# Performance work log

Hardware: AMD Instinct MI355X
Metric: run time of the kernel (lower is better)

## Reference

```python
import jax, jax.numpy as jnp
import numpy as np

B, S, D, H, DK, DV, W = 2, 8192, 1024, 16, 64, 64, 128


def setup_inputs() -> dict:
    key = jax.random.key(0)
    ks = jax.random.split(key, 5)
    scale = 0.02
    x = jax.random.normal(ks[0], (B, S, D), jnp.float32)
    Wq = jax.random.normal(ks[1], (D, H * DK), jnp.float32) * scale
    Wk = jax.random.normal(ks[2], (D, H * DK), jnp.float32) * scale
    Wv = jax.random.normal(ks[3], (D, H * DV), jnp.float32) * scale
    Wo = jax.random.normal(ks[4], (H * DV, D), jnp.float32) * scale
    return {"x": x, "Wq": Wq, "Wk": Wk, "Wv": Wv, "Wo": Wo, "window_size": W}


def _sliding_window_attn(x, Wq, Wk, Wv, Wo, window_size):
    b, s, d = x.shape
    dk = Wq.shape[1] // H
    dv = Wv.shape[1] // H
    Bq = window_size            # block size == band half-width
    nb = s // Bq                # number of query blocks

    # projections -> [B, H, S, dh]
    q = (x @ Wq).reshape(b, s, H, dk).transpose(0, 2, 1, 3)
    k = (x @ Wk).reshape(b, s, H, dk).transpose(0, 2, 1, 3)
    v = (x @ Wv).reshape(b, s, H, dv).transpose(0, 2, 1, 3)

    qb = q.reshape(b, H, nb, Bq, dk)

    # pad keys/values by one block on each side, gather 3-block local context
    kpad = jnp.pad(k, ((0, 0), (0, 0), (Bq, Bq), (0, 0)))
    vpad = jnp.pad(v, ((0, 0), (0, 0), (Bq, Bq), (0, 0)))
    kb = kpad.reshape(b, H, nb + 2, Bq, dk)
    vb = vpad.reshape(b, H, nb + 2, Bq, dv)
    kctx = jnp.concatenate([kb[:, :, :-2], kb[:, :, 1:-1], kb[:, :, 2:]], axis=3)  # [B,H,nb,3Bq,dk]
    vctx = jnp.concatenate([vb[:, :, :-2], vb[:, :, 1:-1], vb[:, :, 2:]], axis=3)  # [B,H,nb,3Bq,dv]

    scores = jnp.einsum("bhnqd,bhnkd->bhnqk", qb, kctx) / jnp.sqrt(jnp.asarray(dk, x.dtype))

    # banded mask: query global idx i = n*Bq + q_loc; key global idx j = (n-1)*Bq + k_loc
    q_loc = jnp.arange(Bq)[:, None]                 # [Bq,1]
    k_rel = jnp.arange(3 * Bq)[None, :] - Bq        # [1,3Bq], offset of j relative to block start
    band = jnp.abs(k_rel - q_loc) <= window_size    # [Bq,3Bq]
    j_global = jnp.arange(nb)[:, None, None] * Bq + k_rel[None]  # [nb,1,3Bq]
    valid = (j_global >= 0) & (j_global < s)
    mask = band[None] & valid                       # [nb,Bq,3Bq]

    neg = jnp.asarray(-1e9, scores.dtype)
    scores = jnp.where(mask[None, None], scores, neg)
    attn = jax.nn.softmax(scores, axis=-1)

    ctx = jnp.einsum("bhnqk,bhnkd->bhnqd", attn, vctx)           # [B,H,nb,Bq,dv]
    ctx = ctx.reshape(b, H, s, dv).transpose(0, 2, 1, 3).reshape(b, s, H * dv)
    return ctx @ Wo


def reference(x, Wq, Wk, Wv, Wo, window_size):
    return _sliding_window_attn(x, Wq, Wk, Wv, Wo, window_size)
```

## Files before the change

### kernel.cpp

```cpp
#include <hip/hip_runtime.h>


typedef __bf16 bf16_t;
typedef bf16_t bf16x8 __attribute__((ext_vector_type(8)));
typedef bf16_t bf16x4 __attribute__((ext_vector_type(4)));
typedef float f32x4 __attribute__((ext_vector_type(4)));

#define CEXP 0.18033688011112042f

__device__ __forceinline__ f32x4 mfma16(bf16x8 a, bf16x8 b, f32x4 c) {
  return __builtin_amdgcn_mfma_f32_16x16x32_bf16(a, b, c, 0, 0, 0);
}

#define GLL16(gptr, lptr)                                                     \
  __builtin_amdgcn_global_load_lds(                                           \
      (__attribute__((address_space(1))) void*)(gptr),                        \
      (__attribute__((address_space(3))) void*)(lptr), 16, 0, 0)

__global__ __launch_bounds__(256) void prep(const float* __restrict__ x,
                                            const float* __restrict__ W0,
                                            const float* __restrict__ W1,
                                            const float* __restrict__ W2,
                                            const float* __restrict__ W3,
                                            bf16_t* __restrict__ xb,
                                            bf16_t* T0, bf16_t* T1,
                                            bf16_t* T2, bf16_t* T3) {
  __shared__ float tile[32][33];
  const int t = threadIdx.x;
  if (blockIdx.x < 8192) {
    int i = blockIdx.x * 256 + t;
    f32x4 a = *(const f32x4*)&x[(size_t)i * 8];
    f32x4 b = *(const f32x4*)&x[(size_t)i * 8 + 4];
    bf16x8 o;
#pragma unroll
    for (int j = 0; j < 4; ++j) { o[j] = (bf16_t)a[j]; o[4 + j] = (bf16_t)b[j]; }
    *(bf16x8*)&xb[(size_t)i * 8] = o;
    return;
  }
  int wb = blockIdx.x - 8192;
  int z = wb >> 10, rem = wb & 1023;
  int bx = rem & 31, by = rem >> 5;
  const float* W; bf16_t* T;
  switch (z) {
    case 0: W = W0; T = T0; break;
    case 1: W = W1; T = T1; break;
    case 2: W = W2; T = T2; break;
    default: W = W3; T = T3; break;
  }
  int tx = t & 31, ty = t >> 5;
  int xc = bx * 32 + tx;
  int y0 = by * 32;
#pragma unroll
  for (int i = ty; i < 32; i += 8) tile[i][tx] = W[(size_t)(y0 + i) * 1024 + xc];
  __syncthreads();
  int xo = y0 + tx;
  int yo = bx * 32;
#pragma unroll
  for (int i = ty; i < 32; i += 8)
    T[(size_t)(yo + i) * 1024 + xo] = (bf16_t)tile[tx][i];
}

__device__ __forceinline__ void gemm256_loop(const bf16_t* __restrict__ A,
                                             const bf16_t* __restrict__ Bt,
                                             int m0, int n0,
                                             bf16_t (*As)[8192],
                                             bf16_t (*Bs)[8192],
                                             f32x4 acc[8][4]) {
  const int K = 1024, NT = 32;
  const int t = threadIdx.x, l = t & 63, w = t >> 6;
  const int fr = l & 15, quad = l >> 4;
  const int wm = w >> 2, wn = w & 3;
  const int srow = w * 16 + (l >> 2);
  const int scol = ((l & 3) ^ ((l >> 3) & 3)) << 3;
  const bf16_t* Asrc = A + (size_t)(m0 + srow) * K + scol;
  const bf16_t* Bsrc = Bt + (size_t)(n0 + srow) * K + scol;
  const size_t cstep = (size_t)128 * K;
  const int sdst = w * 512 + l * 8;
  const int rdoff = fr * 32 + ((quad ^ ((fr >> 1) & 3)) << 3);
  const int abase = wm * 4096 + rdoff;
  const int bbase = wn * 2048 + rdoff;

#pragma unroll
  for (int tt = 0; tt < 2; ++tt) {
    GLL16(Asrc + tt * 32, &As[tt][sdst]);
    GLL16(Asrc + cstep + tt * 32, &As[tt][4096 + sdst]);
    GLL16(Bsrc + tt * 32, &Bs[tt][sdst]);
    GLL16(Bsrc + cstep + tt * 32, &Bs[tt][4096 + sdst]);
  }
  asm volatile("s_waitcnt vmcnt(4)" ::: "memory");
  __builtin_amdgcn_s_barrier();

  for (int tk = 0; tk < NT; ++tk) {
    const int slot = tk & 3;
    const bf16_t* Ap = As[slot];
    const bf16_t* Bp = Bs[slot];
    const bool st = (tk + 2 < NT);
    const int s2 = (tk + 2) & 3;
    __builtin_amdgcn_sched_barrier(0);
    bf16x8 bq[4], af[4];
#pragma unroll
    for (int j = 0; j < 4; ++j) bq[j] = *(const bf16x8*)&Bp[bbase + j * 512];
#pragma unroll
    for (int i = 0; i < 4; ++i) af[i] = *(const bf16x8*)&Ap[abase + i * 512];
    if (st) {
      GLL16(Asrc + (tk + 2) * 32, &As[s2][sdst]);
      GLL16(Asrc + cstep + (tk + 2) * 32, &As[s2][4096 + sdst]);
    }
    __builtin_amdgcn_s_barrier();
    __builtin_amdgcn_s_setprio(1);
#pragma unroll
    for (int i = 0; i < 4; ++i)
#pragma unroll
      for (int j = 0; j < 4; ++j) acc[i][j] = mfma16(af[i], bq[j], acc[i][j]);
    __builtin_amdgcn_s_setprio(0);
    __builtin_amdgcn_s_barrier();
    __builtin_amdgcn_sched_barrier(0);
#pragma unroll
    for (int i = 0; i < 4; ++i) af[i] = *(const bf16x8*)&Ap[abase + (4 + i) * 512];
    if (st) {
      GLL16(Bsrc + (tk + 2) * 32, &Bs[s2][sdst]);
      GLL16(Bsrc + cstep + (tk + 2) * 32, &Bs[s2][4096 + sdst]);
      asm volatile("s_waitcnt vmcnt(4)" ::: "memory");
    } else {
      asm volatile("s_waitcnt vmcnt(0)" ::: "memory");
    }
    __builtin_amdgcn_s_barrier();
    __builtin_amdgcn_s_setprio(1);
#pragma unroll
    for (int i = 0; i < 4; ++i)
#pragma unroll
      for (int j = 0; j < 4; ++j) acc[4 + i][j] = mfma16(af[i], bq[j], acc[4 + i][j]);
    __builtin_amdgcn_s_setprio(0);
    __builtin_amdgcn_s_barrier();
  }
}

__global__ __launch_bounds__(512, 2) void gemm_qkv(const bf16_t* __restrict__ A,
                                                   const bf16_t* __restrict__ Bt,
                                                   bf16_t* __restrict__ qh,
                                                   bf16_t* __restrict__ kh,
                                                   bf16_t* __restrict__ vT2) {
  __shared__ bf16_t As[4][8192];
  __shared__ bf16_t Bs[4][8192];
  const int id = blockIdx.y * 12 + blockIdx.x;
  const int swz = (id & 7) * 96 + (id >> 3);
  const int m0 = (swz / 12) << 8, n0 = (swz % 12) << 8;

  f32x4 acc[8][4] = {};
  gemm256_loop(A, Bt, m0, n0, As, Bs, acc);

  const int t = threadIdx.x, l = t & 63, w = t >> 6;
  const int fr = l & 15, quad = l >> 4;
  const int wm = w >> 2, wn = w & 3;
  const int colbase = n0 + wn * 64;
  if (colbase < 2048) {
    bf16_t* dst = (colbase < 1024) ? qh : kh;
    const int cb = colbase & 1023;
#pragma unroll
    for (int i = 0; i < 8; ++i)
#pragma unroll
      for (int j = 0; j < 4; ++j) {
        int col = cb + j * 16 + fr;
        int h = col >> 6, dk = col & 63;
#pragma unroll
        for (int r = 0; r < 4; ++r) {
          int cm = m0 + wm * 128 + i * 16 + quad * 4 + r;
          int b = cm >> 13, s = cm & 8191;
          dst[((((size_t)(b * 16 + h) << 13) | s) << 6) | dk] = (bf16_t)acc[i][j][r];
        }
      }
  } else {
    const int cb = colbase - 2048;
#pragma unroll
    for (int i = 0; i < 8; ++i) {
      int s0 = m0 + wm * 128 + i * 16;
      int b = s0 >> 13, sblk = (s0 & 8191) >> 4;
#pragma unroll
      for (int j = 0; j < 4; ++j) {
        int col = cb + j * 16;
        int h = col >> 6, dv = (col & 63) + fr;
        bf16x4 pk;
#pragma unroll
        for (int r = 0; r < 4; ++r) pk[r] = (bf16_t)acc[i][j][r];
        *(bf16x4*)&vT2[((size_t)(b * 16 + h) * 512 + sblk) * 1024 + dv * 16 + quad * 4] = pk;
      }
    }
  }
}

__global__ __launch_bounds__(512, 2) void gemm_bt(const bf16_t* __restrict__ A,
                                                  const bf16_t* __restrict__ Bt,
                                                  float* __restrict__ Cf) {
  __shared__ bf16_t As[4][8192];
  __shared__ bf16_t Bs[4][8192];
  const int id = blockIdx.y * 4 + blockIdx.x;
  const int swz = (id & 7) * 32 + (id >> 3);
  const int m0 = (swz >> 2) << 8, n0 = (swz & 3) << 8;

  f32x4 acc[8][4] = {};
  gemm256_loop(A, Bt, m0, n0, As, Bs, acc);

  const int t = threadIdx.x, l = t & 63, w = t >> 6;
  const int fr = l & 15, quad = l >> 4;
  const int wm = w >> 2, wn = w & 3;
#pragma unroll
  for (int i = 0; i < 8; ++i)
#pragma unroll
    for (int j = 0; j < 4; ++j)
#pragma unroll
      for (int r = 0; r < 4; ++r) {
        int cm = m0 + wm * 128 + i * 16 + quad * 4 + r;
        int cn = n0 + wn * 64 + j * 16 + fr;
        Cf[(size_t)cm * 1024 + cn] = acc[i][j][r];
      }
}

#define SKK 72
#define SVS 136
#define PST 136

__global__ __launch_bounds__(256, 3) void swa(const bf16_t* __restrict__ qh,
                                              const bf16_t* __restrict__ kh,
                                              const bf16_t* __restrict__ vT2,
                                              bf16_t* __restrict__ ctx) {
  __shared__ bf16_t Ks[128 * SKK];
  __shared__ bf16_t Vs[64 * SVS];
  __shared__ bf16_t PsT[4][16 * PST];

  const int t = threadIdx.x, lane = t & 63, w = t >> 6;
  const int n = blockIdx.x, h = blockIdx.y, b = blockIdx.z;
  const int fr = lane & 15, quad = lane >> 4, fk = quad << 3;
  const size_t bh = (size_t)(b * 16 + h);

  bf16x8 aq[2][2];
  {
    const size_t qbase = (bh * 8192 + n * 128 + w * 32) * 64;
#pragma unroll
    for (int qt = 0; qt < 2; ++qt)
#pragma unroll
      for (int ks = 0; ks < 2; ++ks)
        aq[qt][ks] = *(const bf16x8*)&qh[qbase + (size_t)(qt * 16 + fr) * 64 + ks * 32 + fk];
  }

  bf16x8 kr[4], vr[4];
  auto loadKV = [&](int kn) {
#pragma unroll
    for (int it = 0; it < 4; ++it) {
      int c = it * 256 + t;
      kr[it] = *(const bf16x8*)&kh[(bh * 8192 + kn * 128 + (c >> 3)) * 64 + ((c & 7) << 3)];
      int sb = c >> 7, dv = (c & 127) >> 1, sh = c & 1;
      vr[it] = *(const bf16x8*)&vT2[(bh * 512 + kn * 8 + sb) * 1024 + dv * 16 + sh * 8];
    }
  };

  const int cbeg = (n == 0) ? 1 : 0;
  const int cend = (n == 63) ? 1 : 2;
  loadKV(n + cbeg - 1);

  float lrow[2] = {0.f, 0.f};
  f32x4 o[2][4] = {};

  for (int ch = cbeg; ch <= cend; ++ch) {
    __syncthreads();
#pragma unroll
    for (int it = 0; it < 4; ++it) {
      int c = it * 256 + t;
      *(bf16x8*)&Ks[(c >> 3) * SKK + ((c & 7) << 3)] = kr[it];
      int sb = c >> 7, dv = (c & 127) >> 1, sh = c & 1;
      *(bf16x8*)&Vs[dv * SVS + sb * 16 + sh * 8] = vr[it];
    }
    __syncthreads();
    if (ch < cend) loadKV(n + ch);

#pragma unroll
    for (int qt = 0; qt < 2; ++qt) {
      const int lo = (ch == 0) ? 2 * w + qt : 0;
      const int hi = (ch == 2) ? 2 * w + qt : 7;

      f32x4 st[8];
      __builtin_amdgcn_s_setprio(1);
#pragma unroll
      for (int kt = 0; kt < 8; ++kt) {
        if (kt < lo || kt > hi) continue;
        bf16x8 k0 = *(const bf16x8*)&Ks[(kt * 16 + fr) * SKK + fk];
        bf16x8 k1 = *(const bf16x8*)&Ks[(kt * 16 + fr) * SKK + 32 + fk];
        st[kt] = mfma16(k1, aq[qt][1], mfma16(k0, aq[qt][0], (f32x4){0.f, 0.f, 0.f, 0.f}));
      }
      __builtin_amdgcn_s_setprio(0);

#pragma unroll
      for (int kt = 0; kt < 8; ++kt) {
        if (kt < lo || kt > hi) continue;
        const bool dL = (ch == 0) && (kt == lo);
        const bool dR = (ch == 2) && (kt == hi);
        bf16x4 pk;
#pragma unroll
        for (int r = 0; r < 4; ++r) {
          float p = exp2f(st[kt][r] * CEXP);
          int kl = quad * 4 + r;
          if (dL) p = (kl >= fr) ? p : 0.f;
          if (dR) p = (kl <= fr) ? p : 0.f;
          lrow[qt] += p;
          pk[r] = (bf16_t)p;
        }
        *(bf16x4*)&PsT[w][fr * PST + kt * 16 + quad * 4] = pk;
      }
      if ((ch == 0) && (lo & 1)) {
        bf16x4 zz; zz[0] = zz[1] = zz[2] = zz[3] = (bf16_t)0.f;
        *(bf16x4*)&PsT[w][fr * PST + (lo - 1) * 16 + quad * 4] = zz;
      }
      if ((ch == 2) && !(hi & 1)) {
        bf16x4 zz; zz[0] = zz[1] = zz[2] = zz[3] = (bf16_t)0.f;
        *(bf16x4*)&PsT[w][fr * PST + (hi + 1) * 16 + quad * 4] = zz;
      }

      const int pl = lo >> 1, ph = hi >> 1;
      __builtin_amdgcn_s_setprio(1);
#pragma unroll
      for (int ks = 0; ks < 4; ++ks) {
        if (ks < pl || ks > ph) continue;
        bf16x8 pa = *(const bf16x8*)&PsT[w][fr * PST + ks * 32 + fk];
#pragma unroll
        for (int dt = 0; dt < 4; ++dt) {
          bf16x8 bv = *(const bf16x8*)&Vs[(dt * 16 + fr) * SVS + ks * 32 + fk];
          o[qt][dt] = mfma16(pa, bv, o[qt][dt]);
        }
      }
      __builtin_amdgcn_s_setprio(0);
    }
  }

#pragma unroll
  for (int qt = 0; qt < 2; ++qt) {
    lrow[qt] += __shfl_xor(lrow[qt], 16, 64);
    lrow[qt] += __shfl_xor(lrow[qt], 32, 64);
  }
  float ln[2][4];
#pragma unroll
  for (int qt = 0; qt < 2; ++qt)
#pragma unroll
    for (int r = 0; r < 4; ++r)
      ln[qt][r] = __shfl(lrow[qt], quad * 4 + r, 64);

#pragma unroll
  for (int qt = 0; qt < 2; ++qt)
#pragma unroll
    for (int dt = 0; dt < 4; ++dt)
#pragma unroll
      for (int r = 0; r < 4; ++r) {
        float ov = o[qt][dt][r] / ln[qt][r];
        int srow = n * 128 + w * 32 + qt * 16 + quad * 4 + r;
        ctx[((size_t)b * 8192 + srow) * 1024 + h * 64 + dt * 16 + fr] = (bf16_t)ov;
      }
}

extern "C" void kernel_launch(void* const* d_in, const int* in_sizes, int n_in,
                              void* d_out, int out_size, void* d_ws, size_t ws_size,
                              hipStream_t stream) {
  const float* x  = (const float*)d_in[0];
  const float* Wq = (const float*)d_in[1];
  const float* Wk = (const float*)d_in[2];
  const float* Wv = (const float*)d_in[3];
  const float* Wo = (const float*)d_in[4];
  float* out = (float*)d_out;

  char* p = (char*)d_ws;
  bf16_t* xb    = (bf16_t*)p; p += (size_t)16384 * 1024 * 2;
  bf16_t* WqkvT = (bf16_t*)p; p += (size_t)3 * 1024 * 1024 * 2;
  bf16_t* WoT   = (bf16_t*)p; p += (size_t)1024 * 1024 * 2;
  bf16_t* qhb   = (bf16_t*)p; p += (size_t)16384 * 1024 * 2;
  bf16_t* khb   = (bf16_t*)p; p += (size_t)16384 * 1024 * 2;
  bf16_t* vT2   = (bf16_t*)p; p += (size_t)16384 * 1024 * 2;
  bf16_t* ctx   = (bf16_t*)p; p += (size_t)16384 * 1024 * 2;

  prep<<<12288, 256, 0, stream>>>(x, Wq, Wk, Wv, Wo, xb, WqkvT,
                                  WqkvT + (size_t)1024 * 1024,
                                  WqkvT + (size_t)2 * 1024 * 1024, WoT);
  gemm_qkv<<<dim3(12, 64), 512, 0, stream>>>(xb, WqkvT, qhb, khb, vT2);
  swa<<<dim3(64, 16, 2), 256, 0, stream>>>(qhb, khb, vT2, ctx);
  gemm_bt<<<dim3(4, 64), 512, 0, stream>>>(ctx, WoT, out);
}
```

Baseline: 344.5 us.

## Software-pipeline LDS fragment loads across K-iterations in GEMM main loop

```diff
diff --git a/kernel.cpp b/kernel.cpp
--- a/kernel.cpp
+++ b/kernel.cpp
@@ -90,34 +90,27 @@
   asm volatile("s_waitcnt vmcnt(4)" ::: "memory");
   __builtin_amdgcn_s_barrier();
 
+  bf16x8 bq[4], bq2[4], afA[4], afB[4];
+#pragma unroll
+  for (int j = 0; j < 4; ++j) bq[j] = *(const bf16x8*)&Bs[0][bbase + j * 512];
+#pragma unroll
+  for (int i = 0; i < 4; ++i) afA[i] = *(const bf16x8*)&As[0][abase + i * 512];
+
+#pragma unroll 4
   for (int tk = 0; tk < NT; ++tk) {
-    const int slot = tk & 3;
-    const bf16_t* Ap = As[slot];
-    const bf16_t* Bp = Bs[slot];
-    const bool st = (tk + 2 < NT);
-    const int s2 = (tk + 2) & 3;
-    __builtin_amdgcn_sched_barrier(0);
-    bf16x8 bq[4], af[4];
-#pragma unroll
-    for (int j = 0; j < 4; ++j) bq[j] = *(const bf16x8*)&Bp[bbase + j * 512];
-#pragma unroll
-    for (int i = 0; i < 4; ++i) af[i] = *(const bf16x8*)&Ap[abase + i * 512];
-    if (st) {
+    const bf16_t* Ap = As[tk & 3];
+    __builtin_amdgcn_s_setprio(1);
+#pragma unroll
+    for (int i = 0; i < 4; ++i) afB[i] = *(const bf16x8*)&Ap[abase + (4 + i) * 512];
+#pragma unroll
+    for (int i = 0; i < 4; ++i)
+#pragma unroll
+      for (int j = 0; j < 4; ++j) acc[i][j] = mfma16(afA[i], bq[j], acc[i][j]);
+    __builtin_amdgcn_s_setprio(0);
+    if (tk + 2 < NT) {
+      const int s2 = (tk + 2) & 3;
       GLL16(Asrc + (tk + 2) * 32, &As[s2][sdst]);
       GLL16(Asrc + cstep + (tk + 2) * 32, &As[s2][4096 + sdst]);
-    }
-    __builtin_amdgcn_s_barrier();
-    __builtin_amdgcn_s_setprio(1);
-#pragma unroll
-    for (int i = 0; i < 4; ++i)
-#pragma unroll
-      for (int j = 0; j < 4; ++j) acc[i][j] = mfma16(af[i], bq[j], acc[i][j]);
-    __builtin_amdgcn_s_setprio(0);
-    __builtin_amdgcn_s_barrier();
-    __builtin_amdgcn_sched_barrier(0);
-#pragma unroll
-    for (int i = 0; i < 4; ++i) af[i] = *(const bf16x8*)&Ap[abase + (4 + i) * 512];
-    if (st) {
       GLL16(Bsrc + (tk + 2) * 32, &Bs[s2][sdst]);
       GLL16(Bsrc + cstep + (tk + 2) * 32, &Bs[s2][4096 + sdst]);
       asm volatile("s_waitcnt vmcnt(4)" ::: "memory");
@@ -126,12 +119,22 @@
     }
     __builtin_amdgcn_s_barrier();
     __builtin_amdgcn_s_setprio(1);
+    if (tk + 1 < NT) {
+      const bf16_t* An = As[(tk + 1) & 3];
+      const bf16_t* Bn = Bs[(tk + 1) & 3];
+#pragma unroll
+      for (int j = 0; j < 4; ++j) bq2[j] = *(const bf16x8*)&Bn[bbase + j * 512];
+#pragma unroll
+      for (int i = 0; i < 4; ++i) afA[i] = *(const bf16x8*)&An[abase + i * 512];
+    }
 #pragma unroll
     for (int i = 0; i < 4; ++i)
 #pragma unroll
-      for (int j = 0; j < 4; ++j) acc[4 + i][j] = mfma16(af[i], bq[j], acc[4 + i][j]);
+      for (int j = 0; j < 4; ++j) acc[4 + i][j] = mfma16(afB[i], bq[j], acc[4 + i][j]);
     __builtin_amdgcn_s_setprio(0);
     __builtin_amdgcn_s_barrier();
+#pragma unroll
+    for (int j = 0; j < 4; ++j) bq[j] = bq2[j];
   }
 }
 
```

Result: no change. 341.3 us (-0.9%).
